# Performance work log

Measured on AMD Instinct MI355X. Metric: run time of the kernel, lower is better.

Reference implementation:

```python
import jax, jax.numpy as jnp
import numpy as np

UNITS = 50
FEAT = 128


def setup_inputs() -> dict:
    key = jax.random.key(0)
    ks = jax.random.split(key, 6)
    B, T, F = 512, 1024, FEAT
    inputs = jax.random.normal(ks[0], (B, T, F), dtype=jnp.float32)
    # Keras LSTM params (gate order: i, f, c, o)
    kernel = jax.random.normal(ks[1], (F, 4 * UNITS), dtype=jnp.float32) * 0.05
    rec_kernel = jax.random.normal(ks[2], (UNITS, 4 * UNITS), dtype=jnp.float32) * 0.05
    bias = jnp.concatenate([
        jnp.zeros((UNITS,), jnp.float32),      # i
        jnp.ones((UNITS,), jnp.float32),       # f (unit_forget_bias)
        jnp.zeros((2 * UNITS,), jnp.float32),  # c, o
    ])
    dense_w = jax.random.normal(ks[3], (UNITS, 1), dtype=jnp.float32) * 0.1
    dense_b = jnp.zeros((1,), jnp.float32)
    return {"inputs": inputs, "kernel": kernel, "rec_kernel": rec_kernel,
            "bias": bias, "dense_w": dense_w, "dense_b": dense_b}


def _lstm_last_hidden(x, kernel, rec_kernel, bias):
    # x: [B, T, F] -> scan over time. Inference mode: dropout is identity.
    B = x.shape[0]
    xT = jnp.swapaxes(x, 0, 1)  # [T, B, F]
    h0 = jnp.zeros((B, UNITS), x.dtype)
    c0 = jnp.zeros((B, UNITS), x.dtype)

    def step(carry, x_t):
        h, c = carry
        z = x_t @ kernel + h @ rec_kernel + bias  # [B, 4U]
        i, f, g, o = jnp.split(z, 4, axis=-1)
        i = jax.nn.sigmoid(i)
        f = jax.nn.sigmoid(f)
        o = jax.nn.sigmoid(o)
        c_new = f * c + i * jnp.tanh(g)
        h_new = o * jnp.tanh(c_new)
        return (h_new, c_new), None

    (h_last, _), _ = jax.lax.scan(step, (h0, c0), xT)
    return h_last  # [B, U]


def reference(inputs, kernel, rec_kernel, bias, dense_w, dense_b):
    h = _lstm_last_hidden(inputs, kernel, rec_kernel, bias)
    return h @ dense_w + dense_b  # [B, 1]
```

## Files before the change

### kernel.cpp

```cpp
#include <hip/hip_runtime.h>
#include <math.h>

#define BATCH 512
#define TT    1024
#define FF    128
#define UU    50
#define ZN    200
#define NP    208
#define NT    13
#define MROWS (BATCH * TT)
#define BM    128
#define RPP   8
#define ESTRIDE 212

typedef __attribute__((ext_vector_type(8))) short bhalf8;
typedef __attribute__((ext_vector_type(4))) short bhalf4;
typedef __attribute__((ext_vector_type(4))) float f32x4;
typedef __attribute__((ext_vector_type(2))) float f32x2;

__device__ __forceinline__ float rcp_fast(float x) {
    return __builtin_amdgcn_rcpf(x);
}
__device__ __forceinline__ float sigmoid_fast(float x) {
    return rcp_fast(1.0f + __builtin_amdgcn_exp2f(-1.442695041f * x));
}
__device__ __forceinline__ float tanh_fast(float x) {
    float e = __builtin_amdgcn_exp2f(2.885390082f * x);
    return fmaf(-2.0f, rcp_fast(e + 1.0f), 1.0f);
}
__device__ __forceinline__ unsigned short bf16_rtn(float x) {
    unsigned int u = __float_as_uint(x);
    unsigned int r = u + 0x7FFFu + ((u >> 16) & 1u);
    return (unsigned short)(r >> 16);
}
__device__ __forceinline__ float bf16_f32(unsigned short h) {
    return __uint_as_float(((unsigned int)h) << 16);
}

__global__ void prep_kt_kernel(const float* __restrict__ K,
                               unsigned short* __restrict__ kt_hi,
                               unsigned short* __restrict__ kt_lo) {
    const int c = threadIdx.x;
    if (c >= NP) return;
    for (int k = 0; k < FF; ++k) {
        float v = (c < ZN) ? K[k * ZN + c] : 0.0f;
        unsigned short h = bf16_rtn(v);
        float lo = v - bf16_f32(h);
        kt_hi[c * FF + k] = h;
        kt_lo[c * FF + k] = bf16_rtn(lo);
    }
}

__launch_bounds__(256, 2)
__global__ void xk_mfma_kernel(const float* __restrict__ x,
                               const unsigned short* __restrict__ kt_hi,
                               const unsigned short* __restrict__ kt_lo,
                               const float* __restrict__ bias,
                               float* __restrict__ zx) {
    __shared__ __align__(16) char xlds[2 * BM * FF * 2];

    const int tid = threadIdx.x;
    const size_t rowbase = (size_t)blockIdx.x * BM;
    const float* xb = x + rowbase * FF;

    const float4* gx = (const float4*)xb;
    #pragma unroll
    for (int i = 0; i < 16; ++i) {
        float4 v = gx[tid + 256 * i];
        const int fidx = (tid + 256 * i) * 4;
        const int row = fidx >> 7;
        const int col = fidx & 127;
        unsigned short h0 = bf16_rtn(v.x), h1 = bf16_rtn(v.y),
                       h2 = bf16_rtn(v.z), h3 = bf16_rtn(v.w);
        bhalf4 hv = { (short)h0, (short)h1, (short)h2, (short)h3 };
        bhalf4 lv = { (short)bf16_rtn(v.x - bf16_f32(h0)),
                      (short)bf16_rtn(v.y - bf16_f32(h1)),
                      (short)bf16_rtn(v.z - bf16_f32(h2)),
                      (short)bf16_rtn(v.w - bf16_f32(h3)) };
        const unsigned byte = (unsigned)((row << 8) + (col << 1)) ^ (((unsigned)row & 7u) << 4);
        *(bhalf4*)(xlds + byte)         = hv;
        *(bhalf4*)(xlds + 32768 + byte) = lv;
    }
    __syncthreads();

    const int w = tid >> 6, l = tid & 63;
    const int lrow = l & 15;
    const int lk   = (l >> 4) << 3;

    float bv[NT];
    #pragma unroll
    for (int nt = 0; nt < NT; ++nt) {
        const int cidx = nt * 16 + lrow;
        bv[nt] = (cidx < ZN) ? bias[cidx] : 0.0f;
    }

    f32x4 acc0[NT], acc1[NT];
    #pragma unroll
    for (int nt = 0; nt < NT; ++nt) { acc0[nt] = (f32x4)0.0f; acc1[nt] = (f32x4)0.0f; }

    #pragma unroll
    for (int ks = 0; ks < 4; ++ks) {
        const int kbyte = (ks * 32 + lk) * 2;
        const int row0 = (w << 5) + lrow;
        const int row1 = row0 + 16;
        const unsigned b0 = (unsigned)((row0 << 8) + kbyte) ^ (((unsigned)row0 & 7u) << 4);
        const unsigned b1 = (unsigned)((row1 << 8) + kbyte) ^ (((unsigned)row1 & 7u) << 4);
        bhalf8 aH0 = *(const bhalf8*)(xlds + b0);
        bhalf8 aL0 = *(const bhalf8*)(xlds + 32768 + b0);
        bhalf8 aH1 = *(const bhalf8*)(xlds + b1);
        bhalf8 aL1 = *(const bhalf8*)(xlds + 32768 + b1);
        #pragma unroll
        for (int nt = 0; nt < NT; ++nt) {
            const int col = nt * 16 + lrow;
            const size_t koff = ((size_t)col << 7) + (size_t)(ks * 32 + lk);
            bhalf8 bH = *(const bhalf8*)(kt_hi + koff);
            bhalf8 bL = *(const bhalf8*)(kt_lo + koff);
            acc0[nt] = __builtin_amdgcn_mfma_f32_16x16x32_bf16(aH0, bH, acc0[nt], 0, 0, 0);
            acc0[nt] = __builtin_amdgcn_mfma_f32_16x16x32_bf16(aH0, bL, acc0[nt], 0, 0, 0);
            acc0[nt] = __builtin_amdgcn_mfma_f32_16x16x32_bf16(aL0, bH, acc0[nt], 0, 0, 0);
            acc1[nt] = __builtin_amdgcn_mfma_f32_16x16x32_bf16(aH1, bH, acc1[nt], 0, 0, 0);
            acc1[nt] = __builtin_amdgcn_mfma_f32_16x16x32_bf16(aH1, bL, acc1[nt], 0, 0, 0);
            acc1[nt] = __builtin_amdgcn_mfma_f32_16x16x32_bf16(aL1, bH, acc1[nt], 0, 0, 0);
        }
    }

    float* elds = (float*)xlds;
    const int rsub = (l >> 4) << 2;
    #pragma unroll
    for (int half = 0; half < 2; ++half) {
        __syncthreads();
        if ((w >> 1) == half) {
            const int lr = (w & 1) * 32;
            #pragma unroll
            for (int nt = 0; nt < NT; ++nt) {
                #pragma unroll
                for (int r = 0; r < 4; ++r) {
                    elds[(lr + rsub + r) * ESTRIDE + nt * 16 + lrow]      = acc0[nt][r] + bv[nt];
                    elds[(lr + 16 + rsub + r) * ESTRIDE + nt * 16 + lrow] = acc1[nt][r] + bv[nt];
                }
            }
        }
        __syncthreads();
        for (int f = tid; f < 64 * 50; f += 256) {
            const int row = f / 50;
            const int u = f - row * 50;
            float4 v;
            v.x = elds[row * ESTRIDE + u];
            v.y = elds[row * ESTRIDE + u + 50];
            v.z = elds[row * ESTRIDE + u + 100];
            v.w = elds[row * ESTRIDE + u + 150];
            *(float4*)&zx[(rowbase + half * 64 + row) * ZN + u * 4] = v;
        }
    }
}

#define ISSUE4(DST, T0) do {                                                  \
    _Pragma("unroll")                                                         \
    for (int s = 0; s < 4; ++s) {                                             \
        int tt = (T0) + s; if (tt > TT - 1) tt = TT - 1;                      \
        if (act) DST[s] = *(const float4*)&zp[(size_t)tt * ZN + l * 4];       \
    }                                                                         \
} while (0)

#define STEP9(V) do {                                                         \
    f32x2 acc0 = {(V).x, 0.f}, acc1 = {(V).y, 0.f};                           \
    f32x2 acc2 = {(V).z, 0.f}, acc3 = {(V).w, 0.f};                           \
    _Pragma("unroll")                                                         \
    for (int k4 = 0; k4 < 12; ++k4) {                                         \
        float4 hv = ((const float4*)hbuf)[k4];      \
        f32x2 hp0 = {hv.x, hv.y}, hp1 = {hv.z, hv.w};                         \
        acc0 = __builtin_elementwise_fma(hp0, rr0[2 * k4], acc0);             \
        acc1 = __builtin_elementwise_fma(hp0, rr1[2 * k4], acc1);             \
        acc2 = __builtin_elementwise_fma(hp0, rr2[2 * k4], acc2);             \
        acc3 = __builtin_elementwise_fma(hp0, rr3[2 * k4], acc3);             \
        acc0 = __builtin_elementwise_fma(hp1, rr0[2 * k4 + 1], acc0);         \
        acc1 = __builtin_elementwise_fma(hp1, rr1[2 * k4 + 1], acc1);         \
        acc2 = __builtin_elementwise_fma(hp1, rr2[2 * k4 + 1], acc2);         \
        acc3 = __builtin_elementwise_fma(hp1, rr3[2 * k4 + 1], acc3);         \
    }                                                                         \
    {                                                                         \
        f32x2 hp = ((const f32x2*)hbuf)[24];                \
        acc0 = __builtin_elementwise_fma(hp, rr0[24], acc0);                  \
        acc1 = __builtin_elementwise_fma(hp, rr1[24], acc1);                  \
        acc2 = __builtin_elementwise_fma(hp, rr2[24], acc2);                  \
        acc3 = __builtin_elementwise_fma(hp, rr3[24], acc3);                  \
    }                                                                         \
    float zi = acc0.x + acc0.y, zf = acc1.x + acc1.y;                         \
    float zg = acc2.x + acc2.y, zo = acc3.x + acc3.y;                         \
    float gi = sigmoid_fast(zi), gf = sigmoid_fast(zf);                       \
    float go = sigmoid_fast(zo), gg = tanh_fast(zg);                          \
    c = gf * c + gi * gg;                                                     \
    h = go * tanh_fast(c);                                                    \
    hbuf[l] = h;                                       \
} while (0)

#define STEPS4(SRC) do {                                                      \
    STEP9(SRC[0]); STEP9(SRC[1]); STEP9(SRC[2]); STEP9(SRC[3]);               \
} while (0)

__launch_bounds__(64, 1)
__global__ void lstm_scan10_kernel(const float* __restrict__ zx4,
                                   const float* __restrict__ R,
                                   const float* __restrict__ dw,
                                   const float* __restrict__ db,
                                   float* __restrict__ out) {
    const int l = threadIdx.x;
    const int b = blockIdx.x;
    const bool act = (l < UU);

    __shared__ __align__(16) float hbuf[64];

    f32x2 rr0[25], rr1[25], rr2[25], rr3[25];
    #pragma unroll
    for (int p = 0; p < 25; ++p) {
        if (act) {
            rr0[p] = (f32x2){ R[(2 * p) * ZN + l],       R[(2 * p + 1) * ZN + l] };
            rr1[p] = (f32x2){ R[(2 * p) * ZN + l + 50],  R[(2 * p + 1) * ZN + l + 50] };
            rr2[p] = (f32x2){ R[(2 * p) * ZN + l + 100], R[(2 * p + 1) * ZN + l + 100] };
            rr3[p] = (f32x2){ R[(2 * p) * ZN + l + 150], R[(2 * p + 1) * ZN + l + 150] };
        } else {
            rr0[p] = (f32x2){0.f, 0.f}; rr1[p] = (f32x2){0.f, 0.f};
            rr2[p] = (f32x2){0.f, 0.f}; rr3[p] = (f32x2){0.f, 0.f};
        }
    }
    #pragma unroll
    for (int p = 0; p < 25; ++p)
        asm volatile("" : "+v"(rr0[p]), "+v"(rr1[p]), "+v"(rr2[p]), "+v"(rr3[p]));

    const float dwv = act ? dw[l] : 0.0f;
    const float* zp = zx4 + (size_t)b * TT * ZN;

    hbuf[l] = 0.0f;
    float h = 0.0f, c = 0.0f;

    float4 pf[4], qf[4];
    #pragma unroll
    for (int s = 0; s < 4; ++s) { pf[s] = (float4){0,0,0,0}; qf[s] = (float4){0,0,0,0}; }

    ISSUE4(pf, 0);
    for (int t = 0; t < TT; t += 8) {
        ISSUE4(qf, t + 4);
        STEPS4(pf);
        ISSUE4(pf, t + 8);
        STEPS4(qf);
    }

    float s = act ? h * dwv : 0.0f;
    #pragma unroll
    for (int off = 32; off > 0; off >>= 1) s += __shfl_down(s, off, 64);
    if (l == 0) out[b] = s + db[0];
}

__launch_bounds__(256, 1)
__global__ void xk_gemm_kernel(const float* __restrict__ x,
                               const float* __restrict__ K,
                               const float* __restrict__ bias,
                               float* __restrict__ zx) {
    const int b = blockIdx.x;
    const int j = threadIdx.x;

    __shared__ __align__(16) float xs[2][RPP * FF];

    float kreg[FF];
    float bj = 0.0f;
    if (j < ZN) {
        #pragma unroll
        for (int k = 0; k < FF; ++k) kreg[k] = K[k * ZN + j];
        bj = bias[j];
    }
    const int jpos = (j % UU) * 4 + (j / UU);

    const float* xrow = x + (size_t)b * TT * FF;
    float* zrow = zx + (size_t)b * TT * ZN;

    ((float4*)xs[0])[threadIdx.x] = ((const float4*)xrow)[threadIdx.x];
    __syncthreads();

    const int NPASS = TT / RPP;
    for (int p = 0; p < NPASS; ++p) {
        const int cur = p & 1, nxt = cur ^ 1;
        float4 gxv;
        const bool more = (p + 1) < NPASS;
        if (more) gxv = ((const float4*)(xrow + (size_t)(p + 1) * RPP * FF))[threadIdx.x];

        if (j < ZN) {
            float acc[RPP];
            #pragma unroll
            for (int r = 0; r < RPP; ++r) acc[r] = bj;
            const float4* xb4 = (const float4*)xs[cur];
            #pragma unroll
            for (int k4 = 0; k4 < FF / 4; ++k4) {
                #pragma unroll
                for (int r = 0; r < RPP; ++r) {
                    float4 xv = xb4[r * (FF / 4) + k4];
                    acc[r] = fmaf(xv.x, kreg[4 * k4 + 0], acc[r]);
                    acc[r] = fmaf(xv.y, kreg[4 * k4 + 1], acc[r]);
                    acc[r] = fmaf(xv.z, kreg[4 * k4 + 2], acc[r]);
                    acc[r] = fmaf(xv.w, kreg[4 * k4 + 3], acc[r]);
                }
            }
            float* zpo = zrow + (size_t)p * RPP * ZN + jpos;
            #pragma unroll
            for (int r = 0; r < RPP; ++r) zpo[r * ZN] = acc[r];
        }
        if (more) ((float4*)xs[nxt])[threadIdx.x] = gxv;
        __syncthreads();
    }
}

extern "C" void kernel_launch(void* const* d_in, const int* in_sizes, int n_in,
                              void* d_out, int out_size, void* d_ws, size_t ws_size,
                              hipStream_t stream) {
    const float* x    = (const float*)d_in[0];
    const float* K    = (const float*)d_in[1];
    const float* R    = (const float*)d_in[2];
    const float* bias = (const float*)d_in[3];
    const float* dw   = (const float*)d_in[4];
    const float* db   = (const float*)d_in[5];
    float* out = (float*)d_out;

    const size_t zx_bytes = (size_t)MROWS * ZN * sizeof(float);
    const size_t kt_elems = (size_t)NP * FF;
    const size_t kt_bytes = kt_elems * sizeof(unsigned short);

    if (ws_size >= zx_bytes + 2 * kt_bytes) {
        float* zx = (float*)d_ws;
        unsigned short* kt_hi = (unsigned short*)((char*)d_ws + zx_bytes);
        unsigned short* kt_lo = kt_hi + kt_elems;
        prep_kt_kernel<<<1, 256, 0, stream>>>(K, kt_hi, kt_lo);
        xk_mfma_kernel<<<MROWS / BM, 256, 0, stream>>>(x, kt_hi, kt_lo, bias, zx);
        lstm_scan10_kernel<<<BATCH, 64, 0, stream>>>(zx, R, dw, db, out);
    } else if (ws_size >= zx_bytes) {
        float* zx = (float*)d_ws;
        xk_gemm_kernel<<<BATCH, 256, 0, stream>>>(x, K, bias, zx);
        lstm_scan10_kernel<<<BATCH, 64, 0, stream>>>(zx, R, dw, db, out);
    }
}
```

Measured before the change: 811.3 us.

## Fuse input projection GEMM into LSTM scan with producer/consumer wave specialization

Replaces the separate MFMA input-projection kernel and the scan kernel with one fused kernel per batch row. One wave computes x@K+bias for 32-timestep chunks into double-buffered LDS using split-bf16 MFMA, while the other wave runs the recurrence over the previous chunk. This removes the round trip of the large zx intermediate through global memory. In exchange each block has only two waves, the per-chunk __syncthreads couples the producer to the serial recurrence, and the producer's global reads of x are not staged through LDS.

```diff
diff --git a/kernel.cpp b/kernel.cpp
--- a/kernel.cpp
+++ b/kernel.cpp
@@ -7,14 +7,12 @@
 #define UU    50
 #define ZN    200
 #define NP    208
-#define NT    13
-#define MROWS (BATCH * TT)
-#define BM    128
-#define RPP   8
-#define ESTRIDE 212
+#define NTL   13
+#define CH    32
+#define NCH   32
+#define ZPAD  (CH * ZN + 64)
 
 typedef __attribute__((ext_vector_type(8))) short bhalf8;
-typedef __attribute__((ext_vector_type(4))) short bhalf4;
 typedef __attribute__((ext_vector_type(4))) float f32x4;
 typedef __attribute__((ext_vector_type(2))) float f32x2;
 
@@ -35,6 +33,19 @@
 }
 __device__ __forceinline__ float bf16_f32(unsigned short h) {
     return __uint_as_float(((unsigned int)h) << 16);
+}
+__device__ __forceinline__ void cvt8(const float4 a, const float4 b,
+                                     bhalf8& hi, bhalf8& lo) {
+    float v0 = a.x, v1 = a.y, v2 = a.z, v3 = a.w;
+    float v4 = b.x, v5 = b.y, v6 = b.z, v7 = b.w;
+    unsigned short h0 = bf16_rtn(v0), h1 = bf16_rtn(v1), h2 = bf16_rtn(v2), h3 = bf16_rtn(v3);
+    unsigned short h4 = bf16_rtn(v4), h5 = bf16_rtn(v5), h6 = bf16_rtn(v6), h7 = bf16_rtn(v7);
+    hi[0]=(short)h0; hi[1]=(short)h1; hi[2]=(short)h2; hi[3]=(short)h3;
+    hi[4]=(short)h4; hi[5]=(short)h5; hi[6]=(short)h6; hi[7]=(short)h7;
+    lo[0]=(short)bf16_rtn(v0 - bf16_f32(h0)); lo[1]=(short)bf16_rtn(v1 - bf16_f32(h1));
+    lo[2]=(short)bf16_rtn(v2 - bf16_f32(h2)); lo[3]=(short)bf16_rtn(v3 - bf16_f32(h3));
+    lo[4]=(short)bf16_rtn(v4 - bf16_f32(h4)); lo[5]=(short)bf16_rtn(v5 - bf16_f32(h5));
+    lo[6]=(short)bf16_rtn(v6 - bf16_f32(h6)); lo[7]=(short)bf16_rtn(v7 - bf16_f32(h7));
 }
 
 __global__ void prep_kt_kernel(const float* __restrict__ K,
@@ -51,123 +62,13 @@
     }
 }
 
-__launch_bounds__(256, 2)
-__global__ void xk_mfma_kernel(const float* __restrict__ x,
-                               const unsigned short* __restrict__ kt_hi,
-                               const unsigned short* __restrict__ kt_lo,
-                               const float* __restrict__ bias,
-                               float* __restrict__ zx) {
-    __shared__ __align__(16) char xlds[2 * BM * FF * 2];
-
-    const int tid = threadIdx.x;
-    const size_t rowbase = (size_t)blockIdx.x * BM;
-    const float* xb = x + rowbase * FF;
-
-    const float4* gx = (const float4*)xb;
-    #pragma unroll
-    for (int i = 0; i < 16; ++i) {
-        float4 v = gx[tid + 256 * i];
-        const int fidx = (tid + 256 * i) * 4;
-        const int row = fidx >> 7;
-        const int col = fidx & 127;
-        unsigned short h0 = bf16_rtn(v.x), h1 = bf16_rtn(v.y),
-                       h2 = bf16_rtn(v.z), h3 = bf16_rtn(v.w);
-        bhalf4 hv = { (short)h0, (short)h1, (short)h2, (short)h3 };
-        bhalf4 lv = { (short)bf16_rtn(v.x - bf16_f32(h0)),
-                      (short)bf16_rtn(v.y - bf16_f32(h1)),
-                      (short)bf16_rtn(v.z - bf16_f32(h2)),
-                      (short)bf16_rtn(v.w - bf16_f32(h3)) };
-        const unsigned byte = (unsigned)((row << 8) + (col << 1)) ^ (((unsigned)row & 7u) << 4);
-        *(bhalf4*)(xlds + byte)         = hv;
-        *(bhalf4*)(xlds + 32768 + byte) = lv;
-    }
-    __syncthreads();
-
-    const int w = tid >> 6, l = tid & 63;
-    const int lrow = l & 15;
-    const int lk   = (l >> 4) << 3;
-
-    float bv[NT];
-    #pragma unroll
-    for (int nt = 0; nt < NT; ++nt) {
-        const int cidx = nt * 16 + lrow;
-        bv[nt] = (cidx < ZN) ? bias[cidx] : 0.0f;
-    }
-
-    f32x4 acc0[NT], acc1[NT];
-    #pragma unroll
-    for (int nt = 0; nt < NT; ++nt) { acc0[nt] = (f32x4)0.0f; acc1[nt] = (f32x4)0.0f; }
-
-    #pragma unroll
-    for (int ks = 0; ks < 4; ++ks) {
-        const int kbyte = (ks * 32 + lk) * 2;
-        const int row0 = (w << 5) + lrow;
-        const int row1 = row0 + 16;
-        const unsigned b0 = (unsigned)((row0 << 8) + kbyte) ^ (((unsigned)row0 & 7u) << 4);
-        const unsigned b1 = (unsigned)((row1 << 8) + kbyte) ^ (((unsigned)row1 & 7u) << 4);
-        bhalf8 aH0 = *(const bhalf8*)(xlds + b0);
-        bhalf8 aL0 = *(const bhalf8*)(xlds + 32768 + b0);
-        bhalf8 aH1 = *(const bhalf8*)(xlds + b1);
-        bhalf8 aL1 = *(const bhalf8*)(xlds + 32768 + b1);
-        #pragma unroll
-        for (int nt = 0; nt < NT; ++nt) {
-            const int col = nt * 16 + lrow;
-            const size_t koff = ((size_t)col << 7) + (size_t)(ks * 32 + lk);
-            bhalf8 bH = *(const bhalf8*)(kt_hi + koff);
-            bhalf8 bL = *(const bhalf8*)(kt_lo + koff);
-            acc0[nt] = __builtin_amdgcn_mfma_f32_16x16x32_bf16(aH0, bH, acc0[nt], 0, 0, 0);
-            acc0[nt] = __builtin_amdgcn_mfma_f32_16x16x32_bf16(aH0, bL, acc0[nt], 0, 0, 0);
-            acc0[nt] = __builtin_amdgcn_mfma_f32_16x16x32_bf16(aL0, bH, acc0[nt], 0, 0, 0);
-            acc1[nt] = __builtin_amdgcn_mfma_f32_16x16x32_bf16(aH1, bH, acc1[nt], 0, 0, 0);
-            acc1[nt] = __builtin_amdgcn_mfma_f32_16x16x32_bf16(aH1, bL, acc1[nt], 0, 0, 0);
-            acc1[nt] = __builtin_amdgcn_mfma_f32_16x16x32_bf16(aL1, bH, acc1[nt], 0, 0, 0);
-        }
-    }
-
-    float* elds = (float*)xlds;
-    const int rsub = (l >> 4) << 2;
-    #pragma unroll
-    for (int half = 0; half < 2; ++half) {
-        __syncthreads();
-        if ((w >> 1) == half) {
-            const int lr = (w & 1) * 32;
-            #pragma unroll
-            for (int nt = 0; nt < NT; ++nt) {
-                #pragma unroll
-                for (int r = 0; r < 4; ++r) {
-                    elds[(lr + rsub + r) * ESTRIDE + nt * 16 + lrow]      = acc0[nt][r] + bv[nt];
-                    elds[(lr + 16 + rsub + r) * ESTRIDE + nt * 16 + lrow] = acc1[nt][r] + bv[nt];
-                }
-            }
-        }
-        __syncthreads();
-        for (int f = tid; f < 64 * 50; f += 256) {
-            const int row = f / 50;
-            const int u = f - row * 50;
-            float4 v;
-            v.x = elds[row * ESTRIDE + u];
-            v.y = elds[row * ESTRIDE + u + 50];
-            v.z = elds[row * ESTRIDE + u + 100];
-            v.w = elds[row * ESTRIDE + u + 150];
-            *(float4*)&zx[(rowbase + half * 64 + row) * ZN + u * 4] = v;
-        }
-    }
-}
-
-#define ISSUE4(DST, T0) do {                                                  \
-    _Pragma("unroll")                                                         \
-    for (int s = 0; s < 4; ++s) {                                             \
-        int tt = (T0) + s; if (tt > TT - 1) tt = TT - 1;                      \
-        if (act) DST[s] = *(const float4*)&zp[(size_t)tt * ZN + l * 4];       \
-    }                                                                         \
-} while (0)
-
-#define STEP9(V) do {                                                         \
+
+#define STEPF(V) do {                                                         \
     f32x2 acc0 = {(V).x, 0.f}, acc1 = {(V).y, 0.f};                           \
     f32x2 acc2 = {(V).z, 0.f}, acc3 = {(V).w, 0.f};                           \
     _Pragma("unroll")                                                         \
     for (int k4 = 0; k4 < 12; ++k4) {                                         \
-        float4 hv = ((const float4*)hbuf)[k4];      \
+        float4 hv = ((const float4*)hbuf)[k4];    \
         f32x2 hp0 = {hv.x, hv.y}, hp1 = {hv.z, hv.w};                         \
         acc0 = __builtin_elementwise_fma(hp0, rr0[2 * k4], acc0);             \
         acc1 = __builtin_elementwise_fma(hp0, rr1[2 * k4], acc1);             \
@@ -191,120 +92,134 @@
     float go = sigmoid_fast(zo), gg = tanh_fast(zg);                          \
     c = gf * c + gi * gg;                                                     \
     h = go * tanh_fast(c);                                                    \
-    hbuf[l] = h;                                       \
+    hbuf[l] = h;                                        \
 } while (0)
 
-#define STEPS4(SRC) do {                                                      \
-    STEP9(SRC[0]); STEP9(SRC[1]); STEP9(SRC[2]); STEP9(SRC[3]);               \
+#define READ4(D, R0) do {                                                     \
+    _Pragma("unroll")                                                         \
+    for (int s_ = 0; s_ < 4; ++s_) {                                          \
+        int r_ = (R0) + s_; if (r_ > CH - 1) r_ = CH - 1;                     \
+        D[s_] = *(const float4*)&zb[r_ * ZN + (l << 2)];                      \
+    }                                                                         \
 } while (0)
 
-__launch_bounds__(64, 1)
-__global__ void lstm_scan10_kernel(const float* __restrict__ zx4,
+#define STEP4(S) do { STEPF(S[0]); STEPF(S[1]); STEPF(S[2]); STEPF(S[3]); } while (0)
+
+__launch_bounds__(128, 1)
+__global__ void lstm_fused2_kernel(const float* __restrict__ x,
+                                   const unsigned short* __restrict__ kt_hi,
+                                   const unsigned short* __restrict__ kt_lo,
+                                   const float* __restrict__ bias,
                                    const float* __restrict__ R,
                                    const float* __restrict__ dw,
                                    const float* __restrict__ db,
                                    float* __restrict__ out) {
-    const int l = threadIdx.x;
+    __shared__ __align__(16) float zlds[2][ZPAD];
+    __shared__ __align__(16) float hbuf[64];
+
+    const int tid = threadIdx.x;
+    const int w = tid >> 6;
+    const int l = tid & 63;
     const int b = blockIdx.x;
+    const int lrow = l & 15;
+    const int lk = (l >> 4) << 3;
+    const int rsub = (l >> 4) << 2;
     const bool act = (l < UU);
-
-    __shared__ __align__(16) float hbuf[64];
 
     f32x2 rr0[25], rr1[25], rr2[25], rr3[25];
     #pragma unroll
     for (int p = 0; p < 25; ++p) {
-        if (act) {
-            rr0[p] = (f32x2){ R[(2 * p) * ZN + l],       R[(2 * p + 1) * ZN + l] };
-            rr1[p] = (f32x2){ R[(2 * p) * ZN + l + 50],  R[(2 * p + 1) * ZN + l + 50] };
-            rr2[p] = (f32x2){ R[(2 * p) * ZN + l + 100], R[(2 * p + 1) * ZN + l + 100] };
-            rr3[p] = (f32x2){ R[(2 * p) * ZN + l + 150], R[(2 * p + 1) * ZN + l + 150] };
-        } else {
-            rr0[p] = (f32x2){0.f, 0.f}; rr1[p] = (f32x2){0.f, 0.f};
-            rr2[p] = (f32x2){0.f, 0.f}; rr3[p] = (f32x2){0.f, 0.f};
+        rr0[p] = (f32x2){0.f, 0.f}; rr1[p] = (f32x2){0.f, 0.f};
+        rr2[p] = (f32x2){0.f, 0.f}; rr3[p] = (f32x2){0.f, 0.f};
+    }
+    float dwv = 0.0f;
+    int   pjx[NTL];
+    float bvv[NTL];
+    #pragma unroll
+    for (int nt = 0; nt < NTL; ++nt) { pjx[nt] = -1; bvv[nt] = 0.f; }
+
+    if (w == 0) {
+        #pragma unroll
+        for (int p = 0; p < 25; ++p) {
+            if (act) {
+                rr0[p] = (f32x2){ R[(2*p) * ZN + l],       R[(2*p+1) * ZN + l] };
+                rr1[p] = (f32x2){ R[(2*p) * ZN + l + 50],  R[(2*p+1) * ZN + l + 50] };
+                rr2[p] = (f32x2){ R[(2*p) * ZN + l + 100], R[(2*p+1) * ZN + l + 100] };
+                rr3[p] = (f32x2){ R[(2*p) * ZN + l + 150], R[(2*p+1) * ZN + l + 150] };
+            }
+        }
+        dwv = act ? dw[l] : 0.0f;
+        hbuf[l] = 0.0f;
+    } else {
+        #pragma unroll
+        for (int nt = 0; nt < NTL; ++nt) {
+            const int j = nt * 16 + lrow;
+            if (j < ZN) { pjx[nt] = (j % UU) * 4 + j / UU; bvv[nt] = bias[j]; }
         }
     }
     #pragma unroll
     for (int p = 0; p < 25; ++p)
         asm volatile("" : "+v"(rr0[p]), "+v"(rr1[p]), "+v"(rr2[p]), "+v"(rr3[p]));
 
-    const float dwv = act ? dw[l] : 0.0f;
-    const float* zp = zx4 + (size_t)b * TT * ZN;
-
-    hbuf[l] = 0.0f;
     float h = 0.0f, c = 0.0f;
-
-    float4 pf[4], qf[4];
-    #pragma unroll
-    for (int s = 0; s < 4; ++s) { pf[s] = (float4){0,0,0,0}; qf[s] = (float4){0,0,0,0}; }
-
-    ISSUE4(pf, 0);
-    for (int t = 0; t < TT; t += 8) {
-        ISSUE4(qf, t + 4);
-        STEPS4(pf);
-        ISSUE4(pf, t + 8);
-        STEPS4(qf);
-    }
-
-    float s = act ? h * dwv : 0.0f;
-    #pragma unroll
-    for (int off = 32; off > 0; off >>= 1) s += __shfl_down(s, off, 64);
-    if (l == 0) out[b] = s + db[0];
-}
-
-__launch_bounds__(256, 1)
-__global__ void xk_gemm_kernel(const float* __restrict__ x,
-                               const float* __restrict__ K,
-                               const float* __restrict__ bias,
-                               float* __restrict__ zx) {
-    const int b = blockIdx.x;
-    const int j = threadIdx.x;
-
-    __shared__ __align__(16) float xs[2][RPP * FF];
-
-    float kreg[FF];
-    float bj = 0.0f;
-    if (j < ZN) {
-        #pragma unroll
-        for (int k = 0; k < FF; ++k) kreg[k] = K[k * ZN + j];
-        bj = bias[j];
-    }
-    const int jpos = (j % UU) * 4 + (j / UU);
-
-    const float* xrow = x + (size_t)b * TT * FF;
-    float* zrow = zx + (size_t)b * TT * ZN;
-
-    ((float4*)xs[0])[threadIdx.x] = ((const float4*)xrow)[threadIdx.x];
     __syncthreads();
 
-    const int NPASS = TT / RPP;
-    for (int p = 0; p < NPASS; ++p) {
-        const int cur = p & 1, nxt = cur ^ 1;
-        float4 gxv;
-        const bool more = (p + 1) < NPASS;
-        if (more) gxv = ((const float4*)(xrow + (size_t)(p + 1) * RPP * FF))[threadIdx.x];
-
-        if (j < ZN) {
-            float acc[RPP];
+    for (int it = 0; it <= NCH; ++it) {
+        if (w == 1 && it < NCH) {
+            float* zb = zlds[it & 1];
+            const int T0 = it * CH;
             #pragma unroll
-            for (int r = 0; r < RPP; ++r) acc[r] = bj;
-            const float4* xb4 = (const float4*)xs[cur];
-            #pragma unroll
-            for (int k4 = 0; k4 < FF / 4; ++k4) {
+            for (int mt = 0; mt < 2; ++mt) {
+                f32x4 acc[NTL];
                 #pragma unroll
-                for (int r = 0; r < RPP; ++r) {
-                    float4 xv = xb4[r * (FF / 4) + k4];
-                    acc[r] = fmaf(xv.x, kreg[4 * k4 + 0], acc[r]);
-                    acc[r] = fmaf(xv.y, kreg[4 * k4 + 1], acc[r]);
-                    acc[r] = fmaf(xv.z, kreg[4 * k4 + 2], acc[r]);
-                    acc[r] = fmaf(xv.w, kreg[4 * k4 + 3], acc[r]);
+                for (int nt = 0; nt < NTL; ++nt) acc[nt] = (f32x4)0.0f;
+                #pragma unroll
+                for (int kc = 0; kc < 4; ++kc) {
+                    const float* xr = x + (size_t)((b << 10) + T0 + mt * 16 + lrow) * FF
+                                        + kc * 32 + lk;
+                    float4 a0 = *(const float4*)xr;
+                    float4 a1 = *(const float4*)(xr + 4);
+                    bhalf8 aH, aL;
+                    cvt8(a0, a1, aH, aL);
+                    #pragma unroll
+                    for (int nt = 0; nt < NTL; ++nt) {
+                        const size_t ko = (size_t)(nt * 16 + lrow) * FF + kc * 32 + lk;
+                        bhalf8 bH = *(const bhalf8*)(kt_hi + ko);
+                        bhalf8 bL = *(const bhalf8*)(kt_lo + ko);
+                        acc[nt] = __builtin_amdgcn_mfma_f32_16x16x32_bf16(aH, bH, acc[nt], 0, 0, 0);
+                        acc[nt] = __builtin_amdgcn_mfma_f32_16x16x32_bf16(aH, bL, acc[nt], 0, 0, 0);
+                        acc[nt] = __builtin_amdgcn_mfma_f32_16x16x32_bf16(aL, bH, acc[nt], 0, 0, 0);
+                    }
+                }
+                #pragma unroll
+                for (int nt = 0; nt < NTL; ++nt) {
+                    if (pjx[nt] >= 0) {
+                        #pragma unroll
+                        for (int r = 0; r < 4; ++r)
+                            zb[(mt * 16 + rsub + r) * ZN + pjx[nt]] = acc[nt][r] + bvv[nt];
+                    }
                 }
             }
-            float* zpo = zrow + (size_t)p * RPP * ZN + jpos;
-            #pragma unroll
-            for (int r = 0; r < RPP; ++r) zpo[r * ZN] = acc[r];
-        }
-        if (more) ((float4*)xs[nxt])[threadIdx.x] = gxv;
+        }
+        if (w == 0 && it > 0) {
+            const float* zb = zlds[(it - 1) & 1];
+            float4 sp[4], sq[4];
+            READ4(sp, 0);
+            for (int g = 0; g < 4; ++g) {
+                READ4(sq, 8 * g + 4);
+                STEP4(sp);
+                READ4(sp, 8 * g + 8);
+                STEP4(sq);
+            }
+        }
         __syncthreads();
+    }
+
+    if (w == 0) {
+        float s = act ? h * dwv : 0.0f;
+        #pragma unroll
+        for (int off = 32; off > 0; off >>= 1) s += __shfl_down(s, off, 64);
+        if (l == 0) out[b] = s + db[0];
     }
 }
 
@@ -319,20 +234,10 @@
     const float* db   = (const float*)d_in[5];
     float* out = (float*)d_out;
 
-    const size_t zx_bytes = (size_t)MROWS * ZN * sizeof(float);
     const size_t kt_elems = (size_t)NP * FF;
-    const size_t kt_bytes = kt_elems * sizeof(unsigned short);
-
-    if (ws_size >= zx_bytes + 2 * kt_bytes) {
-        float* zx = (float*)d_ws;
-        unsigned short* kt_hi = (unsigned short*)((char*)d_ws + zx_bytes);
-        unsigned short* kt_lo = kt_hi + kt_elems;
-        prep_kt_kernel<<<1, 256, 0, stream>>>(K, kt_hi, kt_lo);
-        xk_mfma_kernel<<<MROWS / BM, 256, 0, stream>>>(x, kt_hi, kt_lo, bias, zx);
-        lstm_scan10_kernel<<<BATCH, 64, 0, stream>>>(zx, R, dw, db, out);
-    } else if (ws_size >= zx_bytes) {
-        float* zx = (float*)d_ws;
-        xk_gemm_kernel<<<BATCH, 256, 0, stream>>>(x, K, bias, zx);
-        lstm_scan10_kernel<<<BATCH, 64, 0, stream>>>(zx, R, dw, db, out);
-    }
-}
+    unsigned short* kt_hi = (unsigned short*)d_ws;
+    unsigned short* kt_lo = kt_hi + kt_elems;
+
+    prep_kt_kernel<<<1, 256, 0, stream>>>(K, kt_hi, kt_lo);
+    lstm_fused2_kernel<<<BATCH, 128, 0, stream>>>(x, kt_hi, kt_lo, bias, R, dw, db, out);
+}
```

Measured after the change: 971.2 us. 19.7% more time.
